# Kernel tuning notes

Measured on AMD Instinct MI355X. Metric: run time of the kernel, lower is better.

Reference implementation:

```python
import jax, jax.numpy as jnp
import numpy as np

LN_EPS = 1e-5
ALPHA_Q = 1.0

def _ln(t, g, b):
    mu = jnp.mean(t, -1, keepdims=True)
    var = jnp.var(t, -1, keepdims=True)
    return (t - mu) / jnp.sqrt(var + LN_EPS) * g + b

def _mlp(t, w1, b1, w2, b2):
    h = jax.nn.gelu(t @ w1.T + b1, approximate=False)
    return h @ w2.T + b2

def setup_inputs() -> dict:
    key = jax.random.key(0)
    B, N, L, E, H, D = 2, 2048, 2048, 1024, 16, 4
    ks = jax.random.split(key, 40)
    rn = lambda i, shape, sc: jax.random.normal(ks[i], shape, jnp.float32) * sc
    inp = {}
    inp['x'] = rn(0, (B, N, E), 1.0)
    inp['xp'] = jax.random.uniform(ks[1], (B, N, D), jnp.float32)
    inp['y'] = rn(2, (B, L, E), 1.0)
    inp['yp'] = jax.random.uniform(ks[3], (B, L, D), jnp.float32)
    inp['attn_mask'] = jax.random.uniform(ks[4], (1, 1, N, L), jnp.float32)
    # PositionEncoder params (torch Linear convention: weight [out,in])
    inp['p_w1'] = rn(5, (E, D), 1.0 / D)
    inp['p_b1'] = jax.random.uniform(ks[6], (E,), jnp.float32, 0.0, np.pi)
    inp['p_w2'] = rn(7, (E, D), 1.0 / D)
    inp['p_b2'] = jax.random.uniform(ks[8], (E,), jnp.float32, 0.0, np.pi)
    # QueryEncoder: LayerNorm + mlp1 + mlp2 (mlp0 is dead code in the source)
    inp['q_ln_g'] = jnp.ones((E,), jnp.float32); inp['q_ln_b'] = jnp.zeros((E,), jnp.float32)
    inp['q_m1_w1'] = rn(9, (2 * E, E), 0.02); inp['q_m1_b1'] = jnp.zeros((2 * E,), jnp.float32)
    inp['q_m1_w2'] = rn(10, (E, 2 * E), 0.02); inp['q_m1_b2'] = jnp.zeros((E,), jnp.float32)
    inp['q_m2_w1'] = rn(11, (2 * E, E), 0.02); inp['q_m2_b1'] = jnp.zeros((2 * E,), jnp.float32)
    inp['q_m2_w2'] = rn(12, (E, 2 * E), 0.02); inp['q_m2_b2'] = jnp.zeros((E,), jnp.float32)
    # KeyEncoder: LayerNorm + mlp1 (mlp0 dead code)
    inp['k_ln_g'] = jnp.ones((E,), jnp.float32); inp['k_ln_b'] = jnp.zeros((E,), jnp.float32)
    inp['k_m1_w1'] = rn(13, (2 * E, E), 0.02); inp['k_m1_b1'] = jnp.zeros((2 * E,), jnp.float32)
    inp['k_m1_w2'] = rn(14, (E, 2 * E), 0.02); inp['k_m1_b2'] = jnp.zeros((E,), jnp.float32)
    # V: LayerNorm + Linear
    inp['v_ln_g'] = jnp.ones((E,), jnp.float32); inp['v_ln_b'] = jnp.zeros((E,), jnp.float32)
    inp['v_w'] = rn(15, (E, E), 0.02); inp['v_b'] = jnp.zeros((E,), jnp.float32)
    # output projections
    inp['proj1_w'] = rn(16, (E, E), 0.02); inp['proj1_b'] = jnp.zeros((E,), jnp.float32)
    inp['proj2_w'] = rn(17, (E, D * H), 0.02); inp['proj2_b'] = jnp.zeros((E,), jnp.float32)
    return inp

def reference(x, xp, y, yp, attn_mask, p_w1, p_b1, p_w2, p_b2,
              q_ln_g, q_ln_b, q_m1_w1, q_m1_b1, q_m1_w2, q_m1_b2,
              q_m2_w1, q_m2_b1, q_m2_w2, q_m2_b2,
              k_ln_g, k_ln_b, k_m1_w1, k_m1_b1, k_m1_w2, k_m1_b2,
              v_ln_g, v_ln_b, v_w, v_b, proj1_w, proj1_b, proj2_w, proj2_b):
    B, N, E = x.shape
    L = y.shape[1]
    D = xp.shape[2]
    H = proj2_w.shape[1] // D
    C = E // H
    # PositionEncoder: query side with bias, key side without bias
    pxt = ALPHA_Q * xp
    xp1 = pxt @ p_w1.T + p_b1            # [B,N,E]
    xp2 = pxt @ p_w2.T + p_b2
    pyt = ALPHA_Q * yp
    yp1 = pyt @ p_w1.T                   # [B,L,E], no bias
    yp2 = pyt @ p_w2.T
    rh = lambda t: t.reshape(t.shape[0], -1, H, C)
    # QueryEncoder
    xn = _ln(x, q_ln_g, q_ln_b)
    x1 = _mlp(xn, q_m1_w1, q_m1_b1, q_m1_w2, q_m1_b2)
    x2 = _mlp(xn, q_m2_w1, q_m2_b1, q_m2_w2, q_m2_b2)
    q = jnp.concatenate([rh(x1 * jnp.cos(xp1)), rh(x1 * jnp.sin(xp1)),
                         rh(x2 * jnp.cos(xp2)), rh(x2 * jnp.sin(xp2))], axis=-1)  # [B,N,H,4C]
    # KeyEncoder (note: second cos/sin block is the raw position code)
    yn = _ln(y, k_ln_g, k_ln_b)
    y1 = _mlp(yn, k_m1_w1, k_m1_b1, k_m1_w2, k_m1_b2)
    k = jnp.concatenate([rh(y1 * jnp.cos(yp1)), rh(y1 * jnp.sin(yp1)),
                         rh(jnp.cos(yp2)), rh(jnp.sin(yp2))], axis=-1)            # [B,L,H,4C]
    scale = (4 * C) ** (-0.5)
    attn = jax.nn.softmax(jnp.einsum('bnhd,blhd->bhnl', q, k) * scale, axis=-1)
    # masked renormalization (mask applied AFTER softmax)
    eps = min(1e-8, 1.0 / L)
    attn = attn * attn_mask
    attn = attn / (jnp.sum(attn, axis=-1, keepdims=True) + eps)
    # values
    v = (_ln(y, v_ln_g, v_ln_b) @ v_w.T + v_b).reshape(B, L, H, C)
    out1 = jnp.einsum('bhnl,blhc->bnhc', attn, v).reshape(B, N, E) @ proj1_w.T + proj1_b
    out2 = jnp.einsum('bhnl,bld->bnhd', attn, yp) - xp[:, :, None, :]             # [B,N,H,D]
    out2 = out2.reshape(B, N, H * D) @ proj2_w.T + proj2_b
    return (out1 + out2, attn, xp)
```

## Files before the change

### kernel.cpp

```cpp
#include <hip/hip_runtime.h>
#include <math.h>
#include <stdint.h>

#define DEV static __device__ __forceinline__

typedef __bf16 bf16x8 __attribute__((ext_vector_type(8)));
typedef __bf16 bf16x4v __attribute__((ext_vector_type(4)));
typedef float f32x4 __attribute__((ext_vector_type(4)));

constexpr int Nn = 2048, Ll = 2048, Ee = 1024, Hh = 16;
constexpr float SCALE = 0.0625f;

constexpr size_t OFF_XN   = 0;
constexpr size_t OFF_YNK  = 8388608;
constexpr size_t OFF_YNV  = 16777216;
constexpr size_t OFF_H12  = 25165824;
constexpr size_t OFF_H3   = 58720256;
constexpr size_t OFF_X1   = 75497472;
constexpr size_t OFF_X2   = 83886080;
constexpr size_t OFF_Y1   = 92274688;
constexpr size_t OFF_QWS  = 100663296;
constexpr size_t OFF_KWS  = 134217728;
constexpr size_t OFF_VWS  = 167772160;
constexpr size_t OFF_DNV  = 176160768;
constexpr size_t OFF_YPT  = 176422912;
constexpr size_t OFF_MSK  = 176685056;
constexpr size_t OFF_AVZ  = 185073664;
constexpr size_t OFF_W1122= 193986560;
constexpr size_t OFF_W12  = 202375168;
constexpr size_t OFF_W22  = 206569472;
constexpr size_t OFF_WK1  = 210763776;
constexpr size_t OFF_WK2  = 214958080;
constexpr size_t OFF_WV   = 219152384;
constexpr size_t OFF_WP   = 221249536;
constexpr size_t OFF_EM   = 223477760;

DEV void gl2l(const void* g, void* l) {
  __builtin_amdgcn_global_load_lds((const __attribute__((address_space(1))) void*)g,
                                   (__attribute__((address_space(3))) void*)l, 16, 0, 0);
}

DEV float gelu_f(float v) {
  float x = v * 0.70710678118654752f;
  float ax = fabsf(x);
  float t = 1.f / fmaf(0.3275911f, ax, 1.f);
  float y = t * fmaf(t, fmaf(t, fmaf(t, fmaf(t, 1.061405429f, -1.453152027f),
                                     1.421413741f), -0.284496736f), 0.254829592f);
  float er = 1.f - y * __expf(-x * x);
  er = (x < 0.f) ? -er : er;
  return 0.5f * v * (1.f + er);
}

__launch_bounds__(256)
__global__ void prep_ln(const float* __restrict__ s0, const float* __restrict__ s1,
                        const float* __restrict__ s2, const float* __restrict__ s3,
                        const float* __restrict__ s4, const float* __restrict__ s5,
                        const float* __restrict__ s6,
                        __bf16* __restrict__ d0, __bf16* __restrict__ d1,
                        __bf16* __restrict__ d2, __bf16* __restrict__ d3,
                        __bf16* __restrict__ d4, __bf16* __restrict__ d5,
                        __bf16* __restrict__ d6,
                        const float* __restrict__ pw1, const float* __restrict__ pw2,
                        __bf16* __restrict__ wp,
                        const float* __restrict__ mask, __bf16* __restrict__ mb,
                        const float* __restrict__ yp, __bf16* __restrict__ ypT,
                        const float* __restrict__ x, const float* __restrict__ y,
                        const float* __restrict__ qg, const float* __restrict__ qb,
                        const float* __restrict__ kg, const float* __restrict__ kb,
                        const float* __restrict__ vg, const float* __restrict__ vb,
                        __bf16* __restrict__ xn, __bf16* __restrict__ ynk,
                        __bf16* __restrict__ ynv) {
  const int tid = threadIdx.x;
  if (blockIdx.x >= 18512) {
    const int t = blockIdx.x - 18512;
    const bool isx = t < 4096;
    const int row = isx ? t : t - 4096;
    const float* src = (isx ? x : y) + (size_t)row * Ee;
    const float4 v = ((const float4*)src)[tid];
    float s = v.x + v.y + v.z + v.w;
    float q = v.x*v.x + v.y*v.y + v.z*v.z + v.w*v.w;
    #pragma unroll
    for (int o = 32; o > 0; o >>= 1) { s += __shfl_down(s, o); q += __shfl_down(q, o); }
    __shared__ float ls[4], lq[4];
    if ((tid & 63) == 0) { ls[tid >> 6] = s; lq[tid >> 6] = q; }
    __syncthreads();
    s = ls[0] + ls[1] + ls[2] + ls[3];
    q = lq[0] + lq[1] + lq[2] + lq[3];
    const float mu = s * (1.f / Ee);
    const float rstd = rsqrtf(q * (1.f / Ee) - mu * mu + 1e-5f);
    const int e0 = tid << 2;
    float h0 = (v.x - mu) * rstd, h1 = (v.y - mu) * rstd,
          h2 = (v.z - mu) * rstd, h3 = (v.w - mu) * rstd;
    if (isx) {
      bf16x4v o;
      o[0] = (__bf16)(h0 * qg[e0]   + qb[e0]);
      o[1] = (__bf16)(h1 * qg[e0+1] + qb[e0+1]);
      o[2] = (__bf16)(h2 * qg[e0+2] + qb[e0+2]);
      o[3] = (__bf16)(h3 * qg[e0+3] + qb[e0+3]);
      *(bf16x4v*)(xn + (size_t)row * Ee + e0) = o;
    } else {
      bf16x4v ok, ov;
      ok[0] = (__bf16)(h0 * kg[e0]   + kb[e0]);
      ok[1] = (__bf16)(h1 * kg[e0+1] + kb[e0+1]);
      ok[2] = (__bf16)(h2 * kg[e0+2] + kb[e0+2]);
      ok[3] = (__bf16)(h3 * kg[e0+3] + kb[e0+3]);
      ov[0] = (__bf16)(h0 * vg[e0]   + vb[e0]);
      ov[1] = (__bf16)(h1 * vg[e0+1] + vb[e0+1]);
      ov[2] = (__bf16)(h2 * vg[e0+2] + vb[e0+2]);
      ov[3] = (__bf16)(h3 * vg[e0+3] + vb[e0+3]);
      *(bf16x4v*)(ynk + (size_t)row * Ee + e0) = ok;
      *(bf16x4v*)(ynv + (size_t)row * Ee + e0) = ov;
    }
    return;
  }
  int u = blockIdx.x * 256 + tid;
  if (u < 3407872) {
    int seg = u >> 19, r = u & 524287;
    const float* s; __bf16* d;
    if      (seg == 0) { s = s0; d = d0; }
    else if (seg == 1) { s = s1; d = d1; }
    else if (seg == 2) { s = s2; d = d2; }
    else if (seg == 3) { s = s3; d = d3; }
    else if (seg == 4) { s = s4; d = d4; }
    else if (seg == 5) { s = s5; d = d5; }
    else               { s = s6; d = d6; }
    float4 v = ((const float4*)s)[r];
    bf16x4v o; o[0]=(__bf16)v.x; o[1]=(__bf16)v.y; o[2]=(__bf16)v.z; o[3]=(__bf16)v.w;
    ((bf16x4v*)d)[r] = o;
  } else if (u < 3686400) {
    int p = u - 3407872;
    int row = p / 272, c4 = p - row * 272;
    float4 v = (c4 < 256) ? ((const float4*)pw1)[row * 256 + c4]
                          : ((const float4*)pw2)[row * 16 + (c4 - 256)];
    bf16x4v o; o[0]=(__bf16)v.x; o[1]=(__bf16)v.y; o[2]=(__bf16)v.z; o[3]=(__bf16)v.w;
    *(bf16x4v*)(wp + (size_t)row * 1088 + (c4 << 2)) = o;
  } else if (u < 4734976) {
    int q = u - 3686400;
    float4 v = ((const float4*)mask)[q];
    bf16x4v o; o[0]=(__bf16)v.x; o[1]=(__bf16)v.y; o[2]=(__bf16)v.z; o[3]=(__bf16)v.w;
    ((bf16x4v*)mb)[q] = o;
  } else {
    int t0 = (u - 4734976) << 2;
    #pragma unroll
    for (int k = 0; k < 4; k++) {
      int i = t0 + k;
      int b = i >> 13, d = (i >> 11) & 3, l = i & 2047;
      ypT[i] = (__bf16)yp[(((size_t)b << 11) + l) * 4 + d];
    }
  }
}

#define STAGE_A(BM_, A_, lda_, kt_, kh_, buf_)                                        \
  _Pragma("unroll")                                                                   \
  for (int jj = 0; jj < (BM_) / 128; jj++) {                                          \
    int c = (jj << 9) + tid;                                                          \
    int row_ = c >> 2, j_ = c & 3;                                                    \
    int col_ = ((kt_) << 6) + ((kh_) << 5) + ((j_ ^ (row_ & 3)) << 3);                \
    gl2l(A_ + (size_t)(m0 + row_) * (lda_) + col_,                                    \
         As + ((((buf_) << 1) + (kh_)) * ((BM_) * 32)) + (c << 3));                   \
  }

#define STAGE_B(W_, ldw_, kt_, kh_, buf_)                                             \
  _Pragma("unroll")                                                                   \
  for (int jj = 0; jj < 2; jj++) {                                                    \
    int c = (jj << 9) + tid;                                                          \
    int row_ = c >> 2, j_ = c & 3;                                                    \
    int col_ = ((kt_) << 6) + ((kh_) << 5) + ((j_ ^ (row_ & 3)) << 3);                \
    gl2l(W_ + (size_t)(n0 + row_) * (ldw_) + col_,                                    \
         Bs + ((((buf_) << 1) + (kh_)) * 8192) + (c << 3));                           \
  }

#define LOAD_A(BM_, buf_, ks_)                                                        \
  _Pragma("unroll")                                                                   \
  for (int i = 0; i < (BM_) / 32; i++) {                                              \
    int ra = wm + (i << 4) + li;                                                      \
    af[i] = *(const bf16x8*)(As + ((((buf_) << 1) + (ks_)) * ((BM_) * 32))            \
             + ra * 32 + ((g ^ (ra & 3)) << 3));                                      \
  }

#define LOAD_B(buf_, ks_, qn_)                                                        \
  _Pragma("unroll")                                                                   \
  for (int jj = 0; jj < 2; jj++) {                                                    \
    int rb = wn + ((qn_) << 5) + (jj << 4) + li;                                      \
    bw[jj] = *(const bf16x8*)(Bs + ((((buf_) << 1) + (ks_)) * 8192)                   \
             + rb * 32 + ((g ^ (rb & 3)) << 3));                                      \
  }

#define MFMA_Q(BM_, qn_)                                                              \
  __builtin_amdgcn_s_setprio(1);                                                      \
  _Pragma("unroll")                                                                   \
  for (int i = 0; i < (BM_) / 32; i++) {                                              \
    acc[i][((qn_) << 1)]     = __builtin_amdgcn_mfma_f32_16x16x32_bf16(af[i], bw[0], acc[i][((qn_) << 1)], 0, 0, 0);     \
    acc[i][((qn_) << 1) + 1] = __builtin_amdgcn_mfma_f32_16x16x32_bf16(af[i], bw[1], acc[i][((qn_) << 1) + 1], 0, 0, 0); \
  }                                                                                   \
  __builtin_amdgcn_s_setprio(0);

#define PH_SYNC                                                                       \
  __builtin_amdgcn_s_barrier();                                                       \
  asm volatile("s_waitcnt lgkmcnt(0)" ::: "memory");                                  \
  __builtin_amdgcn_sched_barrier(0);

#define PH_END __builtin_amdgcn_s_barrier();

#define GEMM_PIPE(BM_, A_, lda_, W_, ldw_, K_)                                        \
  const int w = tid >> 6, lane = tid & 63, g = lane >> 4, li = lane & 15;             \
  const int wm = (w >> 2) * ((BM_) / 2), wn = (w & 3) << 6;                           \
  constexpr int MI_ = (BM_) / 32;                                                     \
  constexpr int VMC = (BM_) / 128 + 2;                                                \
  f32x4 acc[MI_][4];                                                                  \
  _Pragma("unroll")                                                                   \
  for (int i = 0; i < MI_; i++)                                                       \
    _Pragma("unroll")                                                                 \
    for (int j = 0; j < 4; j++) acc[i][j] = (f32x4)0.f;                               \
  STAGE_A(BM_, A_, lda_, 0, 0, 0) STAGE_B(W_, ldw_, 0, 0, 0)                          \
  STAGE_A(BM_, A_, lda_, 0, 1, 0) STAGE_B(W_, ldw_, 0, 1, 0)                          \
  STAGE_A(BM_, A_, lda_, 1, 0, 1) STAGE_B(W_, ldw_, 1, 0, 1)                          \
  asm volatile("s_waitcnt vmcnt(%0)" :: "i"(VMC) : "memory");                         \
  __builtin_amdgcn_s_barrier();                                                       \
  const int NT = (K_) >> 6;                                                           \
  bf16x8 af[MI_], bw[2];                                                              \
  for (int t = 0; t < NT; t++) {                                                      \
    const int buf = t & 1, nbuf = buf ^ 1;                                            \
    const bool sB = (t + 1 < NT);                                                     \
    const bool sA = (t + 2 < NT);                                                     \
    LOAD_A(BM_, buf, 0) LOAD_B(buf, 0, 0)                                             \
    if (sB) { STAGE_A(BM_, A_, lda_, t + 1, 1, nbuf) }                                \
    PH_SYNC MFMA_Q(BM_, 0) PH_END                                                     \
    LOAD_B(buf, 0, 1)                                                                 \
    if (sB) {                                                                         \
      STAGE_B(W_, ldw_, t + 1, 1, nbuf)                                               \
      asm volatile("s_waitcnt vmcnt(%0)" :: "i"(VMC) : "memory");                     \
    } else {                                                                          \
      asm volatile("s_waitcnt vmcnt(0)" ::: "memory");                                \
    }                                                                                 \
    PH_SYNC MFMA_Q(BM_, 1) PH_END                                                     \
    LOAD_A(BM_, buf, 1) LOAD_B(buf, 1, 0)                                             \
    if (sA) { STAGE_A(BM_, A_, lda_, t + 2, 0, buf) }                                 \
    PH_SYNC MFMA_Q(BM_, 0) PH_END                                                     \
    LOAD_B(buf, 1, 1)                                                                 \
    if (sA) {                                                                         \
      STAGE_B(W_, ldw_, t + 2, 0, buf)                                                \
      asm volatile("s_waitcnt vmcnt(%0)" :: "i"(VMC) : "memory");                     \
    } else if (t + 1 < NT) {                                                          \
      asm volatile("s_waitcnt vmcnt(0)" ::: "memory");                                \
    }                                                                                 \
    PH_SYNC MFMA_Q(BM_, 1) PH_END                                                     \
  }

__launch_bounds__(512, 2)
__global__ void gemm_mlp1(const __bf16* __restrict__ xn, const __bf16* __restrict__ ynk,
                          const __bf16* __restrict__ w1122, const __bf16* __restrict__ wk1,
                          const float* __restrict__ qb1, const float* __restrict__ qb2,
                          const float* __restrict__ kb1,
                          __bf16* __restrict__ h12, __bf16* __restrict__ h3) {
  __shared__ __align__(16) __bf16 As[2 * 2 * 256 * 32];
  __shared__ __align__(16) __bf16 Bs[2 * 2 * 256 * 32];
  const int tid = threadIdx.x, bid = blockIdx.x;
  if (bid < 256) {
    const int m0 = (bid >> 4) << 8, n0 = (bid & 15) << 8;
    GEMM_PIPE(256, xn, 1024, w1122, 1024, 1024)
    #pragma unroll
    for (int j = 0; j < 4; j++) {
      int n = n0 + wn + (j << 4) + li;
      float bias = (n < 2048) ? qb1[n] : qb2[n - 2048];
      #pragma unroll
      for (int i = 0; i < MI_; i++) {
        #pragma unroll
        for (int r = 0; r < 4; r++) {
          int m = m0 + wm + (i << 4) + (g << 2) + r;
          h12[(size_t)m * 4096 + n] = (__bf16)gelu_f(acc[i][j][r] + bias);
        }
      }
    }
  } else {
    const int rr = bid - 256;
    const int m0 = (rr >> 3) << 7, n0 = (rr & 7) << 8;
    GEMM_PIPE(128, ynk, 1024, wk1, 1024, 1024)
    #pragma unroll
    for (int j = 0; j < 4; j++) {
      int n = n0 + wn + (j << 4) + li;
      float bias = kb1[n];
      #pragma unroll
      for (int i = 0; i < MI_; i++) {
        #pragma unroll
        for (int r = 0; r < 4; r++) {
          int m = m0 + wm + (i << 4) + (g << 2) + r;
          h3[(size_t)m * 2048 + n] = (__bf16)gelu_f(acc[i][j][r] + bias);
        }
      }
    }
  }
}

__launch_bounds__(512, 2)
__global__ void gemm_mlp2(const __bf16* __restrict__ h12, const __bf16* __restrict__ h3,
                          const __bf16* __restrict__ ynv,
                          const __bf16* __restrict__ w12, const __bf16* __restrict__ w22,
                          const __bf16* __restrict__ wk2, const __bf16* __restrict__ wv,
                          const float* __restrict__ bx1, const float* __restrict__ bx2,
                          const float* __restrict__ by1, const float* __restrict__ bv,
                          __bf16* __restrict__ x1, __bf16* __restrict__ x2,
                          __bf16* __restrict__ y1, __bf16* __restrict__ vT) {
  __shared__ __align__(16) __bf16 As[2 * 2 * 256 * 32];
  __shared__ __align__(16) __bf16 Bs[2 * 2 * 256 * 32];
  const int tid = threadIdx.x, bid = blockIdx.x;
  const int seg = bid >> 6, rr = bid & 63;
  const int m0 = (rr >> 2) << 8, n0 = (rr & 3) << 8;
  const __bf16* A; const __bf16* W; const float* bias; __bf16* out; int lda, K;
  if      (seg == 0) { A = h12;        lda = 4096; W = w12; bias = bx1; out = x1; K = 2048; }
  else if (seg == 1) { A = h12 + 2048; lda = 4096; W = w22; bias = bx2; out = x2; K = 2048; }
  else if (seg == 2) { A = h3;         lda = 2048; W = wk2; bias = by1; out = y1; K = 2048; }
  else               { A = ynv;        lda = 1024; W = wv;  bias = bv;  out = vT; K = 1024; }
  GEMM_PIPE(256, A, lda, W, K, K)
  #pragma unroll
  for (int j = 0; j < 4; j++) {
    int n = n0 + wn + (j << 4) + li;
    float bs = bias[n];
    #pragma unroll
    for (int i = 0; i < MI_; i++) {
      #pragma unroll
      for (int r = 0; r < 4; r++) {
        int m = m0 + wm + (i << 4) + (g << 2) + r;
        float v = acc[i][j][r] + bs;
        if (seg == 3) {
          int bb = m >> 11, l = m & 2047, hh = n >> 6, cc = n & 63;
          vT[(((size_t)(bb * Hh + hh) * 64 + cc) << 11) + l] = (__bf16)v;
        } else {
          out[(size_t)m * 1024 + n] = (__bf16)v;
        }
      }
    }
  }
}

__launch_bounds__(256)
__global__ void build_qk(const __bf16* __restrict__ x1, const __bf16* __restrict__ x2,
                         const float* __restrict__ xp,
                         const __bf16* __restrict__ y1, const float* __restrict__ yp,
                         const float* __restrict__ pw1, const float* __restrict__ pb1,
                         const float* __restrict__ pw2, const float* __restrict__ pb2,
                         __bf16* __restrict__ q_ws, __bf16* __restrict__ k_ws) {
  const bool isq = blockIdx.x < 2048;
  const int bid = isq ? blockIdx.x : blockIdx.x - 2048;
  const int t = (bid << 1) + (threadIdx.x >> 7);
  const int tl = threadIdx.x & 127;
  const int b = t >> 11, n = t & 2047;
  const int hh = tl >> 3, ch = tl & 7;
  const int e0 = (hh << 6) + (ch << 3);
  const float* pos = isq ? xp : yp;
  const float p0 = pos[(size_t)t*4], p1 = pos[(size_t)t*4+1],
              p2 = pos[(size_t)t*4+2], p3 = pos[(size_t)t*4+3];
  bf16x8 o0, o1, o2, o3;
  if (isq) {
    bf16x8 v1 = *(const bf16x8*)(x1 + (size_t)t * Ee + e0);
    bf16x8 v2 = *(const bf16x8*)(x2 + (size_t)t * Ee + e0);
    #pragma unroll
    for (int sub = 0; sub < 8; sub++) {
      int e = e0 + sub;
      float a1 = pw1[e*4]*p0 + pw1[e*4+1]*p1 + pw1[e*4+2]*p2 + pw1[e*4+3]*p3 + pb1[e];
      float a2 = pw2[e*4]*p0 + pw2[e*4+1]*p1 + pw2[e*4+2]*p2 + pw2[e*4+3]*p3 + pb2[e];
      float s1, c1, s2, c2;
      __sincosf(a1, &s1, &c1); __sincosf(a2, &s2, &c2);
      float xv1 = (float)v1[sub], xv2 = (float)v2[sub];
      o0[sub] = (__bf16)(xv1 * c1); o1[sub] = (__bf16)(xv1 * s1);
      o2[sub] = (__bf16)(xv2 * c2); o3[sub] = (__bf16)(xv2 * s2);
    }
  } else {
    bf16x8 v1 = *(const bf16x8*)(y1 + (size_t)t * Ee + e0);
    #pragma unroll
    for (int sub = 0; sub < 8; sub++) {
      int e = e0 + sub;
      float a1 = pw1[e*4]*p0 + pw1[e*4+1]*p1 + pw1[e*4+2]*p2 + pw1[e*4+3]*p3;
      float a2 = pw2[e*4]*p0 + pw2[e*4+1]*p1 + pw2[e*4+2]*p2 + pw2[e*4+3]*p3;
      float s1, c1, s2, c2;
      __sincosf(a1, &s1, &c1); __sincosf(a2, &s2, &c2);
      float yv = (float)v1[sub];
      o0[sub] = (__bf16)(yv * c1); o1[sub] = (__bf16)(yv * s1);
      o2[sub] = (__bf16)c2;        o3[sub] = (__bf16)s2;
    }
  }
  const int k = n & 7, bc = ch ^ k;
  __bf16* base = (isq ? q_ws : k_ws) + ((((size_t)b * Hh + hh) * Nn + n) << 8);
  *(bf16x8*)(base + ((bc          ) << 3)) = o0;
  *(bf16x8*)(base + (((8  ^ k) ^ ch) << 3)) = o1;
  *(bf16x8*)(base + (((16 ^ k) ^ ch) << 3)) = o2;
  *(bf16x8*)(base + (((24 ^ k) ^ ch) << 3)) = o3;
}

__launch_bounds__(1024, 1)
__global__ void attn_fused(const __bf16* __restrict__ q_ws, const __bf16* __restrict__ k_ws,
                           const __bf16* __restrict__ vT_ws, const __bf16* __restrict__ ypT_g,
                           const __bf16* __restrict__ mask_bf, const float* __restrict__ xp,
                           __bf16* __restrict__ em_g, float* __restrict__ dinv_g,
                           __bf16* __restrict__ avz, float* __restrict__ attn_out,
                           float* __restrict__ xp_out) {
  __shared__ __align__(16) __bf16 kq[2][64 * 256];
  __shared__ __align__(16) __bf16 vt[2][64 * 66];
  __shared__ __align__(16) __bf16 pT[256 * 66];
  __shared__ __align__(16) __bf16 ypl[2][16 * 66];
  __shared__ float te_s[256];
  const int tid = threadIdx.x, w = tid >> 6, lane = tid & 63, g = lane >> 4, li = lane & 15;
  const int logical = ((blockIdx.x & 7) << 5) + (blockIdx.x >> 3);
  const int bh = logical >> 3, nt = logical & 7;
  const int b = bh >> 4, h = bh & 15;
  const int n0 = nt << 8;
  const __bf16* qb = q_ws + (((size_t)bh * Nn + n0) << 8);
  const __bf16* kb = k_ws + (((size_t)bh * Ll) << 8);
  const __bf16* vb = vT_ws + ((size_t)bh << 17);
  const __bf16* yb = ypT_g + ((size_t)b << 13);
  const __bf16* mb = mask_bf + ((size_t)n0 << 11);

  {
    int idx = (blockIdx.x << 6) + (tid & 63);
    if (tid < 64) ((float4*)xp_out)[idx] = ((const float4*)xp)[idx];
  }

  bf16x8 aq[8];
  {
    const int nloc = (w << 4) + li;
    #pragma unroll
    for (int s = 0; s < 8; s++)
      aq[s] = *(const bf16x8*)(qb + ((size_t)nloc << 8) + ((((s << 2) + g) ^ (nloc & 7)) << 3));
  }
  for (int i = tid; i < 1584; i += 1024) {
    int buf = i / 792, idx = i - buf * 792;
    ypl[buf][264 + idx] = (__bf16)0.f;
  }
  {
    bf16x8 vreg; bf16x8 ypreg;
    if (tid < 512) vreg = *(const bf16x8*)(vb + ((size_t)(tid >> 3) << 11) + ((tid & 7) << 3));
    if (tid < 32) ypreg = *(const bf16x8*)(yb + ((size_t)(tid >> 3) << 11) + ((tid & 7) << 3));
    #pragma unroll
    for (int j = 0; j < 2; j++) {
      int c = (j << 10) + tid;
      gl2l(kb + (size_t)(c >> 5) * 256 + ((c & 31) << 3), kq[0] + ((c - lane) << 3));
    }
    if (tid < 512) *(bf16x8*)(vt[0] + (tid >> 3) * 66 + ((tid & 7) << 3)) = vreg;
    if (tid < 32) *(bf16x8*)(ypl[0] + (tid >> 3) * 66 + ((tid & 7) << 3)) = ypreg;
  }
  __syncthreads();

  float se[4] = {0.f, 0.f, 0.f, 0.f};
  float te[2] = {0.f, 0.f};
  f32x4 accv[4]; f32x4 accp;
  #pragma unroll
  for (int cb = 0; cb < 4; cb++) accv[cb] = (f32x4)0.f;
  accp = (f32x4)0.f;

  for (int t = 0; t < 32; ++t) {
    const int l0 = t << 6, cur = t & 1, nxt = cur ^ 1;
    const bool more = (t < 31);
    bf16x8 mk[2];
    #pragma unroll
    for (int j = 0; j < 2; j++) {
      int q = (j << 6) + lane;
      mk[j] = *(const bf16x8*)(mb + (size_t)((w << 4) + (q >> 3)) * 2048 + l0 + ((q & 7) << 3));
    }
    bf16x8 vreg, ypreg;
    if (more) {
      const int l1 = l0 + 64;
      if (tid < 512) vreg = *(const bf16x8*)(vb + ((size_t)(tid >> 3) << 11) + l1 + ((tid & 7) << 3));
      if (tid < 32) ypreg = *(const bf16x8*)(yb + ((size_t)(tid >> 3) << 11) + l1 + ((tid & 7) << 3));
      #pragma unroll
      for (int j = 0; j < 2; j++) {
        int c = (j << 10) + tid;
        gl2l(kb + (size_t)(l1 + (c >> 5)) * 256 + ((c & 31) << 3), kq[nxt] + ((c - lane) << 3));
      }
    }
    f32x4 Cs[4];
    #pragma unroll
    for (int lb = 0; lb < 4; lb++) Cs[lb] = (f32x4)0.f;
    __builtin_amdgcn_s_setprio(1);
    #pragma unroll
    for (int lb = 0; lb < 4; lb++) {
      const int kr = (lb << 4) + li;
      #pragma unroll
      for (int s = 0; s < 8; s++) {
        bf16x8 bk = *(const bf16x8*)(kq[cur] + kr * 256 + ((((s << 2) + g) ^ (kr & 7)) << 3));
        Cs[lb] = __builtin_amdgcn_mfma_f32_16x16x32_bf16(aq[s], bk, Cs[lb], 0, 0, 0);
      }
    }
    __builtin_amdgcn_s_setprio(0);
    #pragma unroll
    for (int lb = 0; lb < 4; lb++) {
      #pragma unroll
      for (int r = 0; r < 4; r++) {
        const int row = (w << 4) + (g << 2) + r;
        float e = __expf(Cs[lb][r] * SCALE);
        se[r] += e;
        pT[row * 66 + (lb << 4) + li] = (__bf16)e;
      }
    }
    asm volatile("s_waitcnt lgkmcnt(0)" ::: "memory");
    __builtin_amdgcn_sched_barrier(0);
    #pragma unroll
    for (int j = 0; j < 2; j++) {
      const int q = (j << 6) + lane;
      const int row = q >> 3, ch = q & 7;
      bf16x8 pv = *(const bf16x8*)(pT + ((w << 4) + row) * 66 + (ch << 3));
      bf16x8 emv;
      float tp = 0.f;
      #pragma unroll
      for (int i = 0; i < 8; i++) {
        float p = (float)pv[i] * (float)mk[j][i];
        emv[i] = (__bf16)p;
        tp += p;
      }
      tp += __shfl_xor(tp, 1);
      tp += __shfl_xor(tp, 2);
      tp += __shfl_xor(tp, 4);
      te[j] += tp;
      *(bf16x8*)(em_g + ((size_t)bh << 22) + ((size_t)(n0 + (w << 4) + row) << 11) + l0 + (ch << 3)) = emv;
      *(bf16x8*)(pT + ((w << 4) + row) * 66 + (ch << 3)) = emv;
    }
    asm volatile("s_waitcnt lgkmcnt(0)" ::: "memory");
    __builtin_amdgcn_sched_barrier(0);
    __builtin_amdgcn_s_setprio(1);
    #pragma unroll
    for (int kc = 0; kc < 2; kc++) {
      bf16x8 vv[4];
      #pragma unroll
      for (int cb = 0; cb < 4; cb++)
        vv[cb] = *(const bf16x8*)(vt[cur] + ((cb << 4) + li) * 66 + (kc << 5) + (g << 3));
      bf16x8 yy = *(const bf16x8*)(ypl[cur] + li * 66 + (kc << 5) + (g << 3));
      bf16x8 pa = *(const bf16x8*)(pT + ((w << 4) + li) * 66 + (kc << 5) + (g << 3));
      #pragma unroll
      for (int cb = 0; cb < 4; cb++)
        accv[cb] = __builtin_amdgcn_mfma_f32_16x16x32_bf16(pa, vv[cb], accv[cb], 0, 0, 0);
      accp = __builtin_amdgcn_mfma_f32_16x16x32_bf16(pa, yy, accp, 0, 0, 0);
    }
    __builtin_amdgcn_s_setprio(0);
    if (more) {
      if (tid < 512) *(bf16x8*)(vt[nxt] + (tid >> 3) * 66 + ((tid & 7) << 3)) = vreg;
      if (tid < 32) *(bf16x8*)(ypl[nxt] + (tid >> 3) * 66 + ((tid & 7) << 3)) = ypreg;
    }
    __syncthreads();
  }

  if ((lane & 7) == 0) {
    #pragma unroll
    for (int j = 0; j < 2; j++)
      te_s[(w << 4) + (j << 3) + (lane >> 3)] = te[j];
  }
  asm volatile("s_waitcnt lgkmcnt(0)" ::: "memory");
  __builtin_amdgcn_sched_barrier(0);
  __syncthreads();

  #pragma unroll
  for (int r = 0; r < 4; r++) {
    float s = se[r];
    #pragma unroll
    for (int o = 1; o < 16; o <<= 1) s += __shfl_xor(s, o);
    float tt = te_s[(w << 4) + (g << 2) + r];
    float dinv = 1.f / (tt + 1e-8f * s);
    const int n = n0 + (w << 4) + (g << 2) + r;
    if (li == 0) {
      dinv_g[((size_t)bh << 11) + n] = dinv;
      te_s[(w << 4) + (g << 2) + r] = dinv;
    }
    #pragma unroll
    for (int cb = 0; cb < 4; cb++)
      avz[((size_t)b * Nn + n) * 1088 + (h << 6) + (cb << 4) + li] = (__bf16)(accv[cb][r] * dinv);
    if (li < 4) {
      float z = accp[r] * dinv - xp[(((size_t)b * Nn + n) << 2) + li];
      avz[((size_t)b * Nn + n) * 1088 + 1024 + (h << 2) + li] = (__bf16)z;
    }
  }
  __syncthreads();

  const __bf16* em_base = em_g + ((size_t)bh << 22) + ((size_t)n0 << 11);
  float* ao_base = attn_out + ((size_t)bh << 22) + ((size_t)n0 << 11);
  for (int p = 0; p < 64; p += 4) {
    bf16x8 v[4]; float dv[4]; int rw[4], chh[4];
    #pragma unroll
    for (int u = 0; u < 4; u++) {
      int c = ((p + u) << 10) + tid;
      rw[u] = c >> 8; chh[u] = c & 255;
      v[u] = *(const bf16x8*)(em_base + ((size_t)rw[u] << 11) + (chh[u] << 3));
      dv[u] = te_s[rw[u]];
    }
    #pragma unroll
    for (int u = 0; u < 4; u++) {
      float4 o0, o1;
      o0.x = (float)v[u][0] * dv[u]; o0.y = (float)v[u][1] * dv[u];
      o0.z = (float)v[u][2] * dv[u]; o0.w = (float)v[u][3] * dv[u];
      o1.x = (float)v[u][4] * dv[u]; o1.y = (float)v[u][5] * dv[u];
      o1.z = (float)v[u][6] * dv[u]; o1.w = (float)v[u][7] * dv[u];
      float* dst = ao_base + ((size_t)rw[u] << 11) + (chh[u] << 3);
      *(float4*)dst = o0;
      *(float4*)(dst + 4) = o1;
    }
  }
}

__launch_bounds__(256)
__global__ void gemm_proj(const __bf16* __restrict__ A, const __bf16* __restrict__ W,
                          const float* __restrict__ bias1, const float* __restrict__ bias2,
                          float* __restrict__ out) {
  constexpr int N = 1024, K = 1088;
  __shared__ __align__(16) __bf16 As[2][128 * 32];
  __shared__ __align__(16) __bf16 Bs[2][64 * 32];
  const int tid = threadIdx.x;
  const int w = tid >> 6, lane = tid & 63, g = lane >> 4, li = lane & 15;
  const int bt = blockIdx.x >> 4;
  const int m0 = bt << 7, n0 = (blockIdx.x & 15) << 6;
  const int wm = (w >> 1) << 6, wn = (w & 1) << 5;
  f32x4 acc[4][2];
  #pragma unroll
  for (int i = 0; i < 4; i++) { acc[i][0] = (f32x4)0.f; acc[i][1] = (f32x4)0.f; }
  auto stage = [&](int buf, int kt) {
    const int col0 = kt << 5;
    #pragma unroll
    for (int j = 0; j < 2; j++) {
      int c = (j << 8) + tid;
      int row = c >> 2, sl = c & 3;
      int col = col0 + ((sl ^ (row & 3)) << 3);
      gl2l(A + (size_t)(m0 + row) * K + col, As[buf] + ((c - lane) << 3));
    }
    {
      int c = tid;
      int row = c >> 2, sl = c & 3;
      int col = col0 + ((sl ^ (row & 3)) << 3);
      gl2l(W + (size_t)(n0 + row) * K + col, Bs[buf] + ((c - lane) << 3));
    }
  };
  const int NT = K >> 5;
  stage(0, 0);
  for (int kt = 0; kt < NT; kt++) {
    const int cur = kt & 1;
    if (kt + 1 < NT) {
      stage(cur ^ 1, kt + 1);
      asm volatile("s_waitcnt vmcnt(3)" ::: "memory");
    } else {
      asm volatile("s_waitcnt vmcnt(0)" ::: "memory");
    }
    __builtin_amdgcn_s_barrier();
    __builtin_amdgcn_sched_barrier(0);
    bf16x8 af[4], bw[2];
    #pragma unroll
    for (int i = 0; i < 4; i++) {
      int ra = wm + (i << 4) + li;
      af[i] = *(const bf16x8*)(As[cur] + ra * 32 + ((g ^ (ra & 3)) << 3));
    }
    #pragma unroll
    for (int j = 0; j < 2; j++) {
      int rb = wn + (j << 4) + li;
      bw[j] = *(const bf16x8*)(Bs[cur] + rb * 32 + ((g ^ (rb & 3)) << 3));
    }
    #pragma unroll
    for (int i = 0; i < 4; i++)
      #pragma unroll
      for (int j = 0; j < 2; j++)
        acc[i][j] = __builtin_amdgcn_mfma_f32_16x16x32_bf16(af[i], bw[j], acc[i][j], 0, 0, 0);
    asm volatile("s_waitcnt lgkmcnt(0)" ::: "memory");
    __builtin_amdgcn_sched_barrier(0);
    __builtin_amdgcn_s_barrier();
  }
  #pragma unroll
  for (int j = 0; j < 2; j++) {
    int n = n0 + wn + (j << 4) + li;
    float bias = bias1[n] + bias2[n];
    #pragma unroll
    for (int i = 0; i < 4; i++) {
      #pragma unroll
      for (int r = 0; r < 4; r++) {
        int m = m0 + wm + (i << 4) + (g << 2) + r;
        out[(size_t)m * N + n] = acc[i][j][r] + bias;
      }
    }
  }
}

extern "C" void kernel_launch(void* const* d_in, const int* in_sizes, int n_in,
                              void* d_out, int out_size, void* d_ws, size_t ws_size,
                              hipStream_t stream) {
  (void)in_sizes; (void)n_in; (void)out_size; (void)ws_size;
  const float* x       = (const float*)d_in[0];
  const float* xp      = (const float*)d_in[1];
  const float* y       = (const float*)d_in[2];
  const float* yp      = (const float*)d_in[3];
  const float* mask    = (const float*)d_in[4];
  const float* p_w1    = (const float*)d_in[5];
  const float* p_b1    = (const float*)d_in[6];
  const float* p_w2    = (const float*)d_in[7];
  const float* p_b2    = (const float*)d_in[8];
  const float* q_ln_g  = (const float*)d_in[9];
  const float* q_ln_b  = (const float*)d_in[10];
  const float* q_m1_w1 = (const float*)d_in[11];
  const float* q_m1_b1 = (const float*)d_in[12];
  const float* q_m1_w2 = (const float*)d_in[13];
  const float* q_m1_b2 = (const float*)d_in[14];
  const float* q_m2_w1 = (const float*)d_in[15];
  const float* q_m2_b1 = (const float*)d_in[16];
  const float* q_m2_w2 = (const float*)d_in[17];
  const float* q_m2_b2 = (const float*)d_in[18];
  const float* k_ln_g  = (const float*)d_in[19];
  const float* k_ln_b  = (const float*)d_in[20];
  const float* k_m1_w1 = (const float*)d_in[21];
  const float* k_m1_b1 = (const float*)d_in[22];
  const float* k_m1_w2 = (const float*)d_in[23];
  const float* k_m1_b2 = (const float*)d_in[24];
  const float* v_ln_g  = (const float*)d_in[25];
  const float* v_ln_b  = (const float*)d_in[26];
  const float* v_w     = (const float*)d_in[27];
  const float* v_b     = (const float*)d_in[28];
  const float* proj1_w = (const float*)d_in[29];
  const float* proj1_b = (const float*)d_in[30];
  const float* proj2_w = (const float*)d_in[31];
  const float* proj2_b = (const float*)d_in[32];

  char* ws = (char*)d_ws;
  __bf16* xn    = (__bf16*)(ws + OFF_XN);
  __bf16* ynk   = (__bf16*)(ws + OFF_YNK);
  __bf16* ynv   = (__bf16*)(ws + OFF_YNV);
  __bf16* h12   = (__bf16*)(ws + OFF_H12);
  __bf16* h3    = (__bf16*)(ws + OFF_H3);
  __bf16* x1    = (__bf16*)(ws + OFF_X1);
  __bf16* x2    = (__bf16*)(ws + OFF_X2);
  __bf16* y1    = (__bf16*)(ws + OFF_Y1);
  __bf16* q_ws  = (__bf16*)(ws + OFF_QWS);
  __bf16* k_ws  = (__bf16*)(ws + OFF_KWS);
  __bf16* vT_ws = (__bf16*)(ws + OFF_VWS);
  float*  dinv  = (float*)(ws + OFF_DNV);
  __bf16* ypT   = (__bf16*)(ws + OFF_YPT);
  __bf16* mskb  = (__bf16*)(ws + OFF_MSK);
  __bf16* avz   = (__bf16*)(ws + OFF_AVZ);
  __bf16* w1122 = (__bf16*)(ws + OFF_W1122);
  __bf16* w12   = (__bf16*)(ws + OFF_W12);
  __bf16* w22   = (__bf16*)(ws + OFF_W22);
  __bf16* wk1   = (__bf16*)(ws + OFF_WK1);
  __bf16* wk2   = (__bf16*)(ws + OFF_WK2);
  __bf16* wv    = (__bf16*)(ws + OFF_WV);
  __bf16* wp    = (__bf16*)(ws + OFF_WP);
  __bf16* em    = (__bf16*)(ws + OFF_EM);

  float* out0     = (float*)d_out;
  float* attn_out = out0 + (size_t)4194304;
  float* xp_out   = out0 + (size_t)138412032;

  prep_ln<<<26704, 256, 0, stream>>>(q_m1_w1, q_m2_w1, q_m1_w2, q_m2_w2, k_m1_w1, k_m1_w2, v_w,
                                     w1122, w1122 + 2097152, w12, w22, wk1, wk2, wv,
                                     proj1_w, proj2_w, wp, mask, mskb, yp, ypT,
                                     x, y, q_ln_g, q_ln_b, k_ln_g, k_ln_b, v_ln_g, v_ln_b,
                                     xn, ynk, ynv);
  gemm_mlp1<<<512, 512, 0, stream>>>(xn, ynk, w1122, wk1, q_m1_b1, q_m2_b1, k_m1_b1, h12, h3);
  gemm_mlp2<<<256, 512, 0, stream>>>(h12, h3, ynv, w12, w22, wk2, wv,
                                     q_m1_b2, q_m2_b2, k_m1_b2, v_b, x1, x2, y1, vT_ws);
  build_qk<<<4096, 256, 0, stream>>>(x1, x2, xp, y1, yp, p_w1, p_b1, p_w2, p_b2, q_ws, k_ws);
  attn_fused<<<256, 1024, 0, stream>>>(q_ws, k_ws, vT_ws, ypT, mskb, xp, em, dinv, avz,
                                       attn_out, xp_out);
  gemm_proj<<<512, 256, 0, stream>>>(avz, wp, proj1_b, proj2_b, out0);
}
```

Measured before the change: 716.3 us.

## Shrink attention blocks to 128 rows and drop LDS double buffering for occupancy

Changes the fused attention kernel from 256 blocks of 1024 threads (256 query rows each) to 512 blocks of 512 threads (128 query rows each), with launch bounds aimed at several resident blocks per CU. The K/V/yp double buffers are removed: tiles are loaded synchronously at the top of each iteration and followed by a barrier, so the kernel relies on overlap between co-resident blocks instead of software prefetch. LDS row padding changes from 66 to 72, setprio hints are dropped, and the epilogue loop loses its manual unrolling. The risks are that K tiles get reloaded twice as often across blocks, there is an extra barrier per iteration, and register limits from the tighter launch bounds could cause spills.

```diff
diff --git a/kernel.cpp b/kernel.cpp
--- a/kernel.cpp
+++ b/kernel.cpp
@@ -387,23 +387,23 @@
   *(bf16x8*)(base + (((24 ^ k) ^ ch) << 3)) = o3;
 }
 
-__launch_bounds__(1024, 1)
+__launch_bounds__(512, 4)
 __global__ void attn_fused(const __bf16* __restrict__ q_ws, const __bf16* __restrict__ k_ws,
                            const __bf16* __restrict__ vT_ws, const __bf16* __restrict__ ypT_g,
                            const __bf16* __restrict__ mask_bf, const float* __restrict__ xp,
                            __bf16* __restrict__ em_g, float* __restrict__ dinv_g,
                            __bf16* __restrict__ avz, float* __restrict__ attn_out,
                            float* __restrict__ xp_out) {
-  __shared__ __align__(16) __bf16 kq[2][64 * 256];
-  __shared__ __align__(16) __bf16 vt[2][64 * 66];
-  __shared__ __align__(16) __bf16 pT[256 * 66];
-  __shared__ __align__(16) __bf16 ypl[2][16 * 66];
-  __shared__ float te_s[256];
+  __shared__ __align__(16) __bf16 kq[64 * 256];
+  __shared__ __align__(16) __bf16 vt[64 * 72];
+  __shared__ __align__(16) __bf16 pT[128 * 72];
+  __shared__ __align__(16) __bf16 ypl[16 * 72];
+  __shared__ float te_s[128];
   const int tid = threadIdx.x, w = tid >> 6, lane = tid & 63, g = lane >> 4, li = lane & 15;
-  const int logical = ((blockIdx.x & 7) << 5) + (blockIdx.x >> 3);
-  const int bh = logical >> 3, nt = logical & 7;
+  const int logical = ((blockIdx.x & 7) << 6) + (blockIdx.x >> 3);
+  const int bh = logical >> 4, nt = logical & 15;
   const int b = bh >> 4, h = bh & 15;
-  const int n0 = nt << 8;
+  const int n0 = nt << 7;
   const __bf16* qb = q_ws + (((size_t)bh * Nn + n0) << 8);
   const __bf16* kb = k_ws + (((size_t)bh * Ll) << 8);
   const __bf16* vb = vT_ws + ((size_t)bh << 17);
@@ -411,8 +411,8 @@
   const __bf16* mb = mask_bf + ((size_t)n0 << 11);
 
   {
-    int idx = (blockIdx.x << 6) + (tid & 63);
-    if (tid < 64) ((float4*)xp_out)[idx] = ((const float4*)xp)[idx];
+    int idx = (blockIdx.x << 5) + (tid & 31);
+    if (tid < 32) ((float4*)xp_out)[idx] = ((const float4*)xp)[idx];
   }
 
   bf16x8 aq[8];
@@ -422,22 +422,7 @@
     for (int s = 0; s < 8; s++)
       aq[s] = *(const bf16x8*)(qb + ((size_t)nloc << 8) + ((((s << 2) + g) ^ (nloc & 7)) << 3));
   }
-  for (int i = tid; i < 1584; i += 1024) {
-    int buf = i / 792, idx = i - buf * 792;
-    ypl[buf][264 + idx] = (__bf16)0.f;
-  }
-  {
-    bf16x8 vreg; bf16x8 ypreg;
-    if (tid < 512) vreg = *(const bf16x8*)(vb + ((size_t)(tid >> 3) << 11) + ((tid & 7) << 3));
-    if (tid < 32) ypreg = *(const bf16x8*)(yb + ((size_t)(tid >> 3) << 11) + ((tid & 7) << 3));
-    #pragma unroll
-    for (int j = 0; j < 2; j++) {
-      int c = (j << 10) + tid;
-      gl2l(kb + (size_t)(c >> 5) * 256 + ((c & 31) << 3), kq[0] + ((c - lane) << 3));
-    }
-    if (tid < 512) *(bf16x8*)(vt[0] + (tid >> 3) * 66 + ((tid & 7) << 3)) = vreg;
-    if (tid < 32) *(bf16x8*)(ypl[0] + (tid >> 3) * 66 + ((tid & 7) << 3)) = ypreg;
-  }
+  for (int i = tid; i < 864; i += 512) ypl[288 + i] = (__bf16)0.f;
   __syncthreads();
 
   float se[4] = {0.f, 0.f, 0.f, 0.f};
@@ -448,39 +433,37 @@
   accp = (f32x4)0.f;
 
   for (int t = 0; t < 32; ++t) {
-    const int l0 = t << 6, cur = t & 1, nxt = cur ^ 1;
-    const bool more = (t < 31);
+    const int l0 = t << 6;
+    bf16x8 vreg = *(const bf16x8*)(vb + ((size_t)(tid >> 3) << 11) + l0 + ((tid & 7) << 3));
+    bf16x8 ypreg;
+    if (tid < 32) ypreg = *(const bf16x8*)(yb + ((size_t)(tid >> 3) << 11) + l0 + ((tid & 7) << 3));
     bf16x8 mk[2];
     #pragma unroll
     for (int j = 0; j < 2; j++) {
       int q = (j << 6) + lane;
       mk[j] = *(const bf16x8*)(mb + (size_t)((w << 4) + (q >> 3)) * 2048 + l0 + ((q & 7) << 3));
     }
-    bf16x8 vreg, ypreg;
-    if (more) {
-      const int l1 = l0 + 64;
-      if (tid < 512) vreg = *(const bf16x8*)(vb + ((size_t)(tid >> 3) << 11) + l1 + ((tid & 7) << 3));
-      if (tid < 32) ypreg = *(const bf16x8*)(yb + ((size_t)(tid >> 3) << 11) + l1 + ((tid & 7) << 3));
-      #pragma unroll
-      for (int j = 0; j < 2; j++) {
-        int c = (j << 10) + tid;
-        gl2l(kb + (size_t)(l1 + (c >> 5)) * 256 + ((c & 31) << 3), kq[nxt] + ((c - lane) << 3));
-      }
-    }
+    #pragma unroll
+    for (int j = 0; j < 4; j++) {
+      int c = (j << 9) + tid;
+      gl2l(kb + (size_t)(l0 + (c >> 5)) * 256 + ((c & 31) << 3), kq + ((c - lane) << 3));
+    }
+    *(bf16x8*)(vt + (tid >> 3) * 72 + ((tid & 7) << 3)) = vreg;
+    if (tid < 32) *(bf16x8*)(ypl + (tid >> 3) * 72 + ((tid & 7) << 3)) = ypreg;
+    __syncthreads();
+
     f32x4 Cs[4];
     #pragma unroll
     for (int lb = 0; lb < 4; lb++) Cs[lb] = (f32x4)0.f;
-    __builtin_amdgcn_s_setprio(1);
     #pragma unroll
     for (int lb = 0; lb < 4; lb++) {
       const int kr = (lb << 4) + li;
       #pragma unroll
       for (int s = 0; s < 8; s++) {
-        bf16x8 bk = *(const bf16x8*)(kq[cur] + kr * 256 + ((((s << 2) + g) ^ (kr & 7)) << 3));
+        bf16x8 bk = *(const bf16x8*)(kq + kr * 256 + ((((s << 2) + g) ^ (kr & 7)) << 3));
         Cs[lb] = __builtin_amdgcn_mfma_f32_16x16x32_bf16(aq[s], bk, Cs[lb], 0, 0, 0);
       }
     }
-    __builtin_amdgcn_s_setprio(0);
     #pragma unroll
     for (int lb = 0; lb < 4; lb++) {
       #pragma unroll
@@ -488,7 +471,7 @@
         const int row = (w << 4) + (g << 2) + r;
         float e = __expf(Cs[lb][r] * SCALE);
         se[r] += e;
-        pT[row * 66 + (lb << 4) + li] = (__bf16)e;
+        pT[row * 72 + (lb << 4) + li] = (__bf16)e;
       }
     }
     asm volatile("s_waitcnt lgkmcnt(0)" ::: "memory");
@@ -497,7 +480,7 @@
     for (int j = 0; j < 2; j++) {
       const int q = (j << 6) + lane;
       const int row = q >> 3, ch = q & 7;
-      bf16x8 pv = *(const bf16x8*)(pT + ((w << 4) + row) * 66 + (ch << 3));
+      bf16x8 pv = *(const bf16x8*)(pT + ((w << 4) + row) * 72 + (ch << 3));
       bf16x8 emv;
       float tp = 0.f;
       #pragma unroll
@@ -511,28 +494,22 @@
       tp += __shfl_xor(tp, 4);
       te[j] += tp;
       *(bf16x8*)(em_g + ((size_t)bh << 22) + ((size_t)(n0 + (w << 4) + row) << 11) + l0 + (ch << 3)) = emv;
-      *(bf16x8*)(pT + ((w << 4) + row) * 66 + (ch << 3)) = emv;
+      *(bf16x8*)(pT + ((w << 4) + row) * 72 + (ch << 3)) = emv;
     }
     asm volatile("s_waitcnt lgkmcnt(0)" ::: "memory");
     __builtin_amdgcn_sched_barrier(0);
-    __builtin_amdgcn_s_setprio(1);
     #pragma unroll
     for (int kc = 0; kc < 2; kc++) {
       bf16x8 vv[4];
       #pragma unroll
       for (int cb = 0; cb < 4; cb++)
-        vv[cb] = *(const bf16x8*)(vt[cur] + ((cb << 4) + li) * 66 + (kc << 5) + (g << 3));
-      bf16x8 yy = *(const bf16x8*)(ypl[cur] + li * 66 + (kc << 5) + (g << 3));
-      bf16x8 pa = *(const bf16x8*)(pT + ((w << 4) + li) * 66 + (kc << 5) + (g << 3));
+        vv[cb] = *(const bf16x8*)(vt + ((cb << 4) + li) * 72 + (kc << 5) + (g << 3));
+      bf16x8 yy = *(const bf16x8*)(ypl + li * 72 + (kc << 5) + (g << 3));
+      bf16x8 pa = *(const bf16x8*)(pT + ((w << 4) + li) * 72 + (kc << 5) + (g << 3));
       #pragma unroll
       for (int cb = 0; cb < 4; cb++)
         accv[cb] = __builtin_amdgcn_mfma_f32_16x16x32_bf16(pa, vv[cb], accv[cb], 0, 0, 0);
       accp = __builtin_amdgcn_mfma_f32_16x16x32_bf16(pa, yy, accp, 0, 0, 0);
-    }
-    __builtin_amdgcn_s_setprio(0);
-    if (more) {
-      if (tid < 512) *(bf16x8*)(vt[nxt] + (tid >> 3) * 66 + ((tid & 7) << 3)) = vreg;
-      if (tid < 32) *(bf16x8*)(ypl[nxt] + (tid >> 3) * 66 + ((tid & 7) << 3)) = ypreg;
     }
     __syncthreads();
   }
@@ -570,26 +547,17 @@
 
   const __bf16* em_base = em_g + ((size_t)bh << 22) + ((size_t)n0 << 11);
   float* ao_base = attn_out + ((size_t)bh << 22) + ((size_t)n0 << 11);
-  for (int p = 0; p < 64; p += 4) {
-    bf16x8 v[4]; float dv[4]; int rw[4], chh[4];
-    #pragma unroll
-    for (int u = 0; u < 4; u++) {
-      int c = ((p + u) << 10) + tid;
-      rw[u] = c >> 8; chh[u] = c & 255;
-      v[u] = *(const bf16x8*)(em_base + ((size_t)rw[u] << 11) + (chh[u] << 3));
-      dv[u] = te_s[rw[u]];
-    }
-    #pragma unroll
-    for (int u = 0; u < 4; u++) {
-      float4 o0, o1;
-      o0.x = (float)v[u][0] * dv[u]; o0.y = (float)v[u][1] * dv[u];
-      o0.z = (float)v[u][2] * dv[u]; o0.w = (float)v[u][3] * dv[u];
-      o1.x = (float)v[u][4] * dv[u]; o1.y = (float)v[u][5] * dv[u];
-      o1.z = (float)v[u][6] * dv[u]; o1.w = (float)v[u][7] * dv[u];
-      float* dst = ao_base + ((size_t)rw[u] << 11) + (chh[u] << 3);
-      *(float4*)dst = o0;
-      *(float4*)(dst + 4) = o1;
-    }
+  for (int p = 0; p < 64; p++) {
+    int c = (p << 9) + tid;
+    int row = c >> 8, ch = c & 255;
+    bf16x8 v = *(const bf16x8*)(em_base + ((size_t)row << 11) + (ch << 3));
+    float dv = te_s[row];
+    float4 o0, o1;
+    o0.x = (float)v[0] * dv; o0.y = (float)v[1] * dv; o0.z = (float)v[2] * dv; o0.w = (float)v[3] * dv;
+    o1.x = (float)v[4] * dv; o1.y = (float)v[5] * dv; o1.z = (float)v[6] * dv; o1.w = (float)v[7] * dv;
+    float* dst = ao_base + ((size_t)row << 11) + (ch << 3);
+    *(float4*)dst = o0;
+    *(float4*)(dst + 4) = o1;
   }
 }
 
@@ -747,7 +715,7 @@
   gemm_mlp2<<<256, 512, 0, stream>>>(h12, h3, ynv, w12, w22, wk2, wv,
                                      q_m1_b2, q_m2_b2, k_m1_b2, v_b, x1, x2, y1, vT_ws);
   build_qk<<<4096, 256, 0, stream>>>(x1, x2, xp, y1, yp, p_w1, p_b1, p_w2, p_b2, q_ws, k_ws);
-  attn_fused<<<256, 1024, 0, stream>>>(q_ws, k_ws, vT_ws, ypT, mskb, xp, em, dinv, avz,
-                                       attn_out, xp_out);
+  attn_fused<<<512, 512, 0, stream>>>(q_ws, k_ws, vT_ws, ypT, mskb, xp, em, dinv, avz,
+                                      attn_out, xp_out);
   gemm_proj<<<512, 256, 0, stream>>>(avz, wp, proj1_b, proj2_b, out0);
 }
```

Result: faster. 666.5 us (-7.0%).
